# Optimization experiments

Measured on AMD Instinct MI355X. Metric: run time of the kernel, lower is better.

## Reference

```python
import jax, jax.numpy as jnp
import numpy as np

B, N, DIM = 2, 2048, 1024
HEADS, DIM_HEAD = 8, 64
INNER = HEADS * DIM_HEAD  # 512
EPS = 1e-5  # fp32 branch of the source LayerNorm


def setup_inputs() -> dict:
    key = jax.random.key(0)
    ks = jax.random.split(key, 5)
    x = jax.random.normal(ks[0], (B, N, DIM), dtype=jnp.float32)
    g = jnp.ones((DIM,), dtype=jnp.float32)  # LayerNorm gain init
    # Linear weights stored as (in, out) so y = x @ W. Source zero-inits
    # to_out; we use small random values so the baseline output is nonzero.
    wq = jax.random.normal(ks[1], (DIM, INNER), dtype=jnp.float32) * 0.02
    wkv = jax.random.normal(ks[2], (DIM, 2 * INNER), dtype=jnp.float32) * 0.02
    wo = jax.random.normal(ks[3], (INNER, DIM), dtype=jnp.float32) * 0.02
    return {"x": x, "g": g, "wq": wq, "wkv": wkv, "wo": wo}


def reference(x, g, wq, wkv, wo):
    # Custom LayerNorm from the source: statistics over dim=1 (sequence axis!)
    mean = jnp.mean(x, axis=1, keepdims=True)
    var = jnp.var(x, axis=1, keepdims=True)  # unbiased=False
    xn = (x - mean) * jax.lax.rsqrt(var + EPS) * g  # g broadcasts on last dim

    q = xn @ wq                      # [b, n, inner]
    kv = xn @ wkv                    # [b, n, 2*inner]
    k, v = jnp.split(kv, 2, axis=-1)

    def split_heads(t):  # b n (h d) -> b h n d
        b, n, _ = t.shape
        return t.reshape(b, n, HEADS, DIM_HEAD).transpose(0, 2, 1, 3)

    q, k, v = map(split_heads, (q, k, v))
    q = q * (DIM_HEAD ** -0.5)

    sim = jnp.einsum('bhid,bhjd->bhij', q, k)   # [b, h, n, n]
    attn = jax.nn.softmax(sim, axis=-1)
    out = jnp.einsum('bhij,bhjd->bhid', attn, v)  # [b, h, n, d]

    out = out.transpose(0, 2, 1, 3).reshape(B, N, INNER)  # b h n d -> b n (h d)
    return out @ wo  # [b, n, dim]
```

## Files before the change

### kernel.cpp

```cpp
#include <hip/hip_runtime.h>
#include <hip/hip_bf16.h>
#include <stdint.h>


#define B_ 2
#define N_ 2048
#define DIM_ 1024
#define DH_ 64
#define INNER_ 512
#define ROWS_ 4096
#define POSTRIDE 2097152
#define BHSTRIDE 131072

#define QSCALE 0.18033688011112042f

typedef __bf16 bf16x8 __attribute__((ext_vector_type(8)));
typedef float floatx4 __attribute__((ext_vector_type(4)));

#if __has_builtin(__builtin_amdgcn_exp2f)
#define EXP2(x) __builtin_amdgcn_exp2f(x)
#else
#define EXP2(x) exp2f(x)
#endif

__device__ __forceinline__ ushort f2bf(float f) {
    union { float f; uint32_t u; } v; v.f = f;
    uint32_t u = v.u;
    u += 0x7fffu + ((u >> 16) & 1u);
    return (ushort)(u >> 16);
}
__device__ __forceinline__ uint32_t pkbf(float a, float b) {
    return (uint32_t)f2bf(a) | ((uint32_t)f2bf(b) << 16);
}
__device__ __forceinline__ size_t frag_off(int m, int k, int nkc) {
    return ((size_t)((m >> 4) * nkc + (k >> 5)) * 64 +
            (size_t)((m & 15) | (((k >> 3) & 3) << 4))) * 8 + (k & 7);
}

__global__ __launch_bounds__(256) void setup_fused(
    const float* __restrict__ x, float* __restrict__ ps, float* __restrict__ pq,
    const float* __restrict__ wq, const float* __restrict__ wkv,
    const float* __restrict__ wo, ushort* __restrict__ wqkv_f,
    ushort* __restrict__ wo_f) {
    __shared__ float tile[32][33];
    int bid = blockIdx.x;
    if (bid < 256) {
        int gd = (bid & 7) * 256 + threadIdx.x;
        int ch = bid >> 3;
        int b = gd >> 10;
        const float* p = x + (size_t)(b * N_ + ch * 64) * DIM_ + (gd & 1023);
        float s = 0.f, q = 0.f;
#pragma unroll 4
        for (int n = 0; n < 64; ++n) { float v = p[(size_t)n * DIM_]; s += v; q += v * v; }
        ps[ch * 2048 + gd] = s;
        pq[ch * 2048 + gd] = q;
        return;
    }
    int t = bid - 256;
    const float* src; ushort* dst; int C, K, k0, ncol0, nglob0; float scale;
    if (t < 512) {
        int kt = t >> 4, nt = t & 15;
        src = wq; dst = wqkv_f; C = 512; K = 1024; scale = QSCALE;
        k0 = kt * 32; ncol0 = nt * 32; nglob0 = ncol0;
    } else if (t < 1536) {
        int u = t - 512; int kt = u >> 5, nt = u & 31;
        src = wkv; dst = wqkv_f; C = 1024; K = 1024; scale = 1.f;
        k0 = kt * 32; ncol0 = nt * 32; nglob0 = 512 + ncol0;
    } else {
        int u = t - 1536; int kt = u >> 5, nt = u & 31;
        src = wo; dst = wo_f; C = 1024; K = 512; scale = 1.f;
        k0 = kt * 32; ncol0 = nt * 32; nglob0 = ncol0;
    }
    int ti = threadIdx.x >> 5, tj = threadIdx.x & 31;
#pragma unroll
    for (int p = 0; p < 4; ++p)
        tile[ti + 8 * p][tj] = src[(size_t)(k0 + ti + 8 * p) * C + ncol0 + tj] * scale;
    __syncthreads();
    if (threadIdx.x < 128) {
        int nl = threadIdx.x & 31, kc8 = threadIdx.x >> 5;
        union { ushort us[8]; uint4 v; } u;
#pragma unroll
        for (int ii = 0; ii < 8; ++ii) u.us[ii] = f2bf(tile[kc8 * 8 + ii][nl]);
        *(uint4*)&dst[frag_off(nglob0 + nl, k0 + kc8 * 8, K >> 5)] = u.v;
    }
}

__global__ __launch_bounds__(256) void finalize_norm(
    const float* __restrict__ ps, const float* __restrict__ pq,
    const float* __restrict__ x, const float* __restrict__ g,
    ushort* __restrict__ xnf) {
    __shared__ float s4[4][64], q4[4][64], aa[64], bb[64];
    int t = threadIdx.x;
    int b = blockIdx.x >> 8, slab = (blockIdx.x >> 4) & 15, nch = blockIdx.x & 15;
    int c0 = slab * 64;
    {
        int c = t & 63, grp = t >> 6;
        float s = 0.f, q = 0.f;
#pragma unroll
        for (int ch = 0; ch < 8; ++ch) {
            int o = (grp * 8 + ch) * 2048 + b * 1024 + c0 + c;
            s += ps[o]; q += pq[o];
        }
        s4[grp][c] = s; q4[grp][c] = q;
    }
    __syncthreads();
    if (t < 64) {
        float s = s4[0][t] + s4[1][t] + s4[2][t] + s4[3][t];
        float q = q4[0][t] + q4[1][t] + q4[2][t] + q4[3][t];
        float mean = s * (1.f / N_);
        float var = q * (1.f / N_) - mean * mean;
        float rstd = rsqrtf(var + 1e-5f);
        float a = rstd * g[c0 + t];
        aa[t] = a; bb[t] = -mean * a;
    }
    __syncthreads();
    int c4 = (t & 15) * 4, ro = t >> 4;
#pragma unroll
    for (int it = 0; it < 8; ++it) {
        int r = nch * 128 + it * 16 + ro;
        int m = b * 2048 + r;
        float4 xv = *(const float4*)&x[(size_t)m * DIM_ + c0 + c4];
        float v0 = xv.x * aa[c4 + 0] + bb[c4 + 0];
        float v1 = xv.y * aa[c4 + 1] + bb[c4 + 1];
        float v2 = xv.z * aa[c4 + 2] + bb[c4 + 2];
        float v3 = xv.w * aa[c4 + 3] + bb[c4 + 3];
        uint2 u; u.x = pkbf(v0, v1); u.y = pkbf(v2, v3);
        *(uint2*)&xnf[frag_off(m, c0 + c4, 32)] = u;
    }
}

template <int NKC>
__device__ __forceinline__ void gemm_core(
    const ushort* __restrict__ pA, const ushort* __restrict__ pB,
    floatx4 (&acc)[4][4]) {
    constexpr int TS = NKC * 512;
    bf16x8 a0[4], b0[4], a1[4], b1[4];
#pragma unroll
    for (int i = 0; i < 4; ++i) {
        a0[i] = *(const bf16x8*)(pA + (size_t)i * TS);
        b0[i] = *(const bf16x8*)(pB + (size_t)i * TS);
    }
    for (int kc = 0; kc < NKC; kc += 2) {
#pragma unroll
        for (int i = 0; i < 4; ++i) {
            a1[i] = *(const bf16x8*)(pA + (size_t)i * TS + (size_t)(kc + 1) * 512);
            b1[i] = *(const bf16x8*)(pB + (size_t)i * TS + (size_t)(kc + 1) * 512);
        }
#pragma unroll
        for (int mi = 0; mi < 4; ++mi)
#pragma unroll
            for (int ni = 0; ni < 4; ++ni)
                acc[mi][ni] = __builtin_amdgcn_mfma_f32_16x16x32_bf16(
                    a0[mi], b0[ni], acc[mi][ni], 0, 0, 0);
        if (kc + 2 < NKC) {
#pragma unroll
            for (int i = 0; i < 4; ++i) {
                a0[i] = *(const bf16x8*)(pA + (size_t)i * TS + (size_t)(kc + 2) * 512);
                b0[i] = *(const bf16x8*)(pB + (size_t)i * TS + (size_t)(kc + 2) * 512);
            }
        }
#pragma unroll
        for (int mi = 0; mi < 4; ++mi)
#pragma unroll
            for (int ni = 0; ni < 4; ++ni)
                acc[mi][ni] = __builtin_amdgcn_mfma_f32_16x16x32_bf16(
                    a1[mi], b1[ni], acc[mi][ni], 0, 0, 0);
    }
}

__global__ __launch_bounds__(128) void gemm_qkv(
    const ushort* __restrict__ xnf, const ushort* __restrict__ wf,
    ushort* __restrict__ qf, ushort* __restrict__ kf, ushort* __restrict__ vf) {
    int tx = threadIdx.x, w = tx >> 6, l = tx & 63;
    int lr = l & 15, lq = l >> 4;
    int bx = blockIdx.x, by = blockIdx.y;
    const ushort* pA = xnf + (size_t)(bx * 4) * 32 * 512 + l * 8;
    const ushort* pB = wf + (size_t)(by * 8 + w * 4) * 32 * 512 + l * 8;
    floatx4 acc[4][4] = {};
    gemm_core<32>(pA, pB, acc);
    int col0 = by * 128 + w * 64;
    int bb2 = (bx * 64) >> 11;
    if (by < 8) {
        ushort* qkbase = (by < 4) ? qf : kf;
#pragma unroll
        for (int ni = 0; ni < 4; ++ni) {
            int col = col0 + 16 * ni + lr;
            int hh = (col >> 6) & 7, d = col & 63;
            ushort* base = qkbase + (size_t)(bb2 * 8 + hh) * BHSTRIDE
                           + (d >> 5) * 512 + ((d >> 3) & 3) * 128 + (d & 7)
                           + (4 * lq) * 8;
#pragma unroll
            for (int mi = 0; mi < 4; ++mi) {
                size_t o2 = (size_t)((bx * 4 + mi) & 127) * 1024;
#pragma unroll
                for (int reg = 0; reg < 4; ++reg)
                    base[o2 + reg * 8] = f2bf(acc[mi][ni][reg]);
            }
        }
    } else {
#pragma unroll
        for (int ni = 0; ni < 4; ++ni) {
            int cv = col0 - 1024 + 16 * ni + lr;
            int hh = cv >> 6, d = cv & 63;
            ushort* base = vf + (size_t)(bb2 * 8 + hh) * BHSTRIDE
                           + (d >> 4) * 32768 + (d & 15) * 8;
#pragma unroll
            for (int mi = 0; mi < 4; ++mi) {
                int nn = (bx * 64 + 16 * mi + 4 * lq) & 2047;
                uint2 u;
                u.x = pkbf(acc[mi][ni][0], acc[mi][ni][1]);
                u.y = pkbf(acc[mi][ni][2], acc[mi][ni][3]);
                *(uint2*)&base[(nn >> 5) * 512 + ((nn >> 3) & 3) * 128 + (nn & 7)] = u;
            }
        }
    }
}

__global__ __launch_bounds__(128) void gemm_out(
    const ushort* __restrict__ af, const ushort* __restrict__ wf,
    float* __restrict__ out) {
    int tx = threadIdx.x, w = tx >> 6, l = tx & 63;
    int lr = l & 15, lq = l >> 4;
    int bx = blockIdx.x, by = blockIdx.y;
    const ushort* pA = af + (size_t)(bx * 4) * 16 * 512 + l * 8;
    const ushort* pB = wf + (size_t)(by * 8 + w * 4) * 16 * 512 + l * 8;
    floatx4 acc[4][4] = {};
    gemm_core<16>(pA, pB, acc);
    int col0 = by * 128 + w * 64;
#pragma unroll
    for (int mi = 0; mi < 4; ++mi)
#pragma unroll
        for (int ni = 0; ni < 4; ++ni) {
            int col = col0 + 16 * ni + lr;
#pragma unroll
            for (int reg = 0; reg < 4; ++reg) {
                int row = bx * 64 + 16 * mi + 4 * lq + reg;
                out[(size_t)row * 1024 + col] = acc[mi][ni][reg];
            }
        }
}

__global__ __launch_bounds__(256, 2) void flash_attn(
    const ushort* __restrict__ qf, const ushort* __restrict__ kf,
    const ushort* __restrict__ vf, float* __restrict__ po,
    float* __restrict__ pl, int nkt) {
    __shared__ __align__(16) ushort sP[4][64 * 72];

    const int tx = threadIdx.x;
    const int w = tx >> 6, l = tx & 63;
    const int lr = l & 15, lq = l >> 4;
    const int qt = blockIdx.x, bh = blockIdx.y, sp = blockIdx.z;
    const int qbase = qt * 256 + w * 64;

    const ushort* qfb = qf + (size_t)bh * BHSTRIDE + (size_t)(qt * 16 + w * 4) * 1024 + l * 8;
    const ushort* kfb = kf + (size_t)bh * BHSTRIDE + (size_t)(sp * nkt * 4) * 1024 + l * 8;
    const ushort* vfb = vf + (size_t)bh * BHSTRIDE + (size_t)(sp * nkt * 2) * 512 + l * 8;
    ushort* sPw = &sP[w][0];

    bf16x8 bq[4][2];
#pragma unroll
    for (int qq = 0; qq < 4; ++qq)
#pragma unroll
        for (int s = 0; s < 2; ++s)
            bq[qq][s] = *(const bf16x8*)(qfb + qq * 1024 + s * 512);

    floatx4 o[4][4] = {};
    float lsum[4] = {0.f, 0.f, 0.f, 0.f};

    bf16x8 ak[8], bv[8];
#pragma unroll
    for (int kk = 0; kk < 4; ++kk) {
        ak[kk * 2 + 0] = *(const bf16x8*)(kfb + kk * 1024);
        ak[kk * 2 + 1] = *(const bf16x8*)(kfb + kk * 1024 + 512);
    }

    for (int kt = 0; kt < nkt; ++kt) {
#pragma unroll
        for (int dt = 0; dt < 4; ++dt) {
            bv[dt * 2 + 0] = *(const bf16x8*)(vfb + dt * 32768 + (kt * 2 + 0) * 512);
            bv[dt * 2 + 1] = *(const bf16x8*)(vfb + dt * 32768 + (kt * 2 + 1) * 512);
        }

        floatx4 c[4][4] = {};
#pragma unroll
        for (int s = 0; s < 2; ++s)
#pragma unroll
            for (int kk = 0; kk < 4; ++kk)
#pragma unroll
                for (int qq = 0; qq < 4; ++qq)
                    c[kk][qq] = __builtin_amdgcn_mfma_f32_16x16x32_bf16(
                        ak[kk * 2 + s], bq[qq][s], c[kk][qq], 0, 0, 0);

        if (kt + 1 < nkt) {
            const ushort* kp = kfb + (size_t)(kt + 1) * 4096;
#pragma unroll
            for (int kk = 0; kk < 4; ++kk) {
                ak[kk * 2 + 0] = *(const bf16x8*)(kp + kk * 1024);
                ak[kk * 2 + 1] = *(const bf16x8*)(kp + kk * 1024 + 512);
            }
        }

#pragma unroll
        for (int kk = 0; kk < 4; ++kk)
#pragma unroll
            for (int qq = 0; qq < 4; ++qq) {
                float e0 = EXP2(c[kk][qq][0]);
                float e1 = EXP2(c[kk][qq][1]);
                float e2 = EXP2(c[kk][qq][2]);
                float e3 = EXP2(c[kk][qq][3]);
                lsum[qq] += (e0 + e1) + (e2 + e3);
                uint2 u; u.x = pkbf(e0, e1); u.y = pkbf(e2, e3);
                *(uint2*)&sPw[(16 * qq + lr) * 72 + 16 * kk + 4 * lq] = u;
            }

#pragma unroll
        for (int s = 0; s < 2; ++s) {
            bf16x8 ap[4];
#pragma unroll
            for (int mi = 0; mi < 4; ++mi)
                ap[mi] = *(const bf16x8*)&sPw[(16 * mi + lr) * 72 + 32 * s + 8 * lq];
#pragma unroll
            for (int mi = 0; mi < 4; ++mi)
#pragma unroll
                for (int dt = 0; dt < 4; ++dt)
                    o[mi][dt] = __builtin_amdgcn_mfma_f32_16x16x32_bf16(
                        ap[mi], bv[dt * 2 + s], o[mi][dt], 0, 0, 0);
        }
    }

#pragma unroll
    for (int qq = 0; qq < 4; ++qq) {
        lsum[qq] += __shfl_xor(lsum[qq], 16);
        lsum[qq] += __shfl_xor(lsum[qq], 32);
    }
    float* pob = po + (size_t)sp * POSTRIDE;
    if (lq == 0) {
#pragma unroll
        for (int qq = 0; qq < 4; ++qq)
            pl[((size_t)sp * 16 + bh) * N_ + qbase + 16 * qq + lr] = lsum[qq];
    }
    const size_t obase = (size_t)bh * N_;
#pragma unroll
    for (int mi = 0; mi < 4; ++mi)
#pragma unroll
        for (int dt = 0; dt < 4; ++dt)
#pragma unroll
            for (int reg = 0; reg < 4; ++reg) {
                int row = qbase + 16 * mi + 4 * lq + reg;
                pob[(obase + row) * DH_ + 16 * dt + lr] = o[mi][dt][reg];
            }
}

__global__ __launch_bounds__(256) void merge_attn(
    const float* __restrict__ po, const float* __restrict__ pl,
    ushort* __restrict__ attnf, int nsplit) {
    int idx = blockIdx.x * 256 + threadIdx.x;
    int d4 = (idx & 15) * 4;
    int h = (idx >> 4) & 7;
    int rowg = idx >> 7;
    int b = rowg >> 11, r = rowg & 2047;
    size_t pbase = ((size_t)b * 8 + h) * N_ + r;
    float4 acc = *(const float4*)&po[pbase * DH_ + d4];
    float lv = pl[pbase];
    for (int s = 1; s < nsplit; ++s) {
        float4 a1 = *(const float4*)&po[(size_t)s * POSTRIDE + pbase * DH_ + d4];
        acc.x += a1.x; acc.y += a1.y; acc.z += a1.z; acc.w += a1.w;
        lv += pl[((size_t)s * 16) * N_ + pbase];
    }
    float inv = 1.f / lv;
    uint2 u;
    u.x = pkbf(acc.x * inv, acc.y * inv);
    u.y = pkbf(acc.z * inv, acc.w * inv);
    *(uint2*)&attnf[frag_off(rowg, h * DH_ + d4, 16)] = u;
}

extern "C" void kernel_launch(void* const* d_in, const int* in_sizes, int n_in,
                              void* d_out, int out_size, void* d_ws, size_t ws_size,
                              hipStream_t stream) {
    const float* x   = (const float*)d_in[0];
    const float* g   = (const float*)d_in[1];
    const float* wq  = (const float*)d_in[2];
    const float* wkv = (const float*)d_in[3];
    const float* wo  = (const float*)d_in[4];
    float* out = (float*)d_out;

    char* ws = (char*)d_ws;
    float*  psum   = (float*)(ws + 0);
    float*  psqr   = (float*)(ws + 262144);
    ushort* xnf    = (ushort*)(ws + 524288);
    ushort* wqkv_f = (ushort*)(ws + 8912896);
    ushort* wo_f   = (ushort*)(ws + 12058624);
    ushort* qfb    = (ushort*)(ws + 13107200);
    ushort* kfb    = (ushort*)(ws + 17301504);
    ushort* vfb    = (ushort*)(ws + 21495808);
    ushort* attnf  = (ushort*)(ws + 25690112);
    float*  plb    = (float*)(ws + 29884416);
    float*  pob    = (float*)(ws + 30408704);

    const int nsplit = (ws_size >= (size_t)66 * 1024 * 1024) ? 4
                     : (ws_size >= (size_t)48 * 1024 * 1024) ? 2 : 1;

    setup_fused<<<2304, 256, 0, stream>>>(x, psum, psqr, wq, wkv, wo, wqkv_f, wo_f);
    finalize_norm<<<512, 256, 0, stream>>>(psum, psqr, x, g, xnf);
    gemm_qkv<<<dim3(64, 12), 128, 0, stream>>>(xnf, wqkv_f, qfb, kfb, vfb);
    flash_attn<<<dim3(8, 16, nsplit), 256, 0, stream>>>(qfb, kfb, vfb, pob, plb, 32 / nsplit);
    merge_attn<<<2048, 256, 0, stream>>>(pob, plb, attnf, nsplit);
    gemm_out<<<dim3(64, 8), 128, 0, stream>>>(attnf, wo_f, out);
}
```

Baseline: 163.2 us.

## Split KV across waves inside flash block and merge partials in LDS

The flash attention kernel now gives each of its four waves a quarter of the key range for the same 64 queries, instead of giving each wave its own query rows and splitting keys across a grid dimension. The partial outputs and row sums are reduced through shared memory and written straight out as normalized bf16, so the separate merge kernel and its fp32 partial buffers in global memory are gone. The GEMM and attention grids are also flattened, with block IDs remapped so that neighbouring tiles land on the same XCD for better L2 reuse. The cost is a larger LDS footprint and a block-wide sync, and each block now does less MFMA work for more reduction overhead.

```diff
diff --git a/kernel.cpp b/kernel.cpp
--- a/kernel.cpp
+++ b/kernel.cpp
@@ -9,7 +9,6 @@
 #define DH_ 64
 #define INNER_ 512
 #define ROWS_ 4096
-#define POSTRIDE 2097152
 #define BHSTRIDE 131072
 
 #define QSCALE 0.18033688011112042f
@@ -173,7 +172,10 @@
     ushort* __restrict__ qf, ushort* __restrict__ kf, ushort* __restrict__ vf) {
     int tx = threadIdx.x, w = tx >> 6, l = tx & 63;
     int lr = l & 15, lq = l >> 4;
-    int bx = blockIdx.x, by = blockIdx.y;
+    int bid = blockIdx.x;
+    int xcd = bid & 7, t = bid >> 3;
+    int bx = xcd * 8 + (t & 7);
+    int by = t >> 3;
     const ushort* pA = xnf + (size_t)(bx * 4) * 32 * 512 + l * 8;
     const ushort* pB = wf + (size_t)(by * 8 + w * 4) * 32 * 512 + l * 8;
     floatx4 acc[4][4] = {};
@@ -221,7 +223,10 @@
     float* __restrict__ out) {
     int tx = threadIdx.x, w = tx >> 6, l = tx & 63;
     int lr = l & 15, lq = l >> 4;
-    int bx = blockIdx.x, by = blockIdx.y;
+    int bid = blockIdx.x;
+    int xcd = bid & 7, t = bid >> 3;
+    int bx = xcd * 8 + (t & 7);
+    int by = t >> 3;
     const ushort* pA = af + (size_t)(bx * 4) * 16 * 512 + l * 8;
     const ushort* pB = wf + (size_t)(by * 8 + w * 4) * 16 * 512 + l * 8;
     floatx4 acc[4][4] = {};
@@ -242,20 +247,21 @@
 
 __global__ __launch_bounds__(256, 2) void flash_attn(
     const ushort* __restrict__ qf, const ushort* __restrict__ kf,
-    const ushort* __restrict__ vf, float* __restrict__ po,
-    float* __restrict__ pl, int nkt) {
-    __shared__ __align__(16) ushort sP[4][64 * 72];
+    const ushort* __restrict__ vf, ushort* __restrict__ attnf) {
+    __shared__ __align__(16) float sArena[4 * 4352];
+    __shared__ float sL[4][64];
 
     const int tx = threadIdx.x;
     const int w = tx >> 6, l = tx & 63;
     const int lr = l & 15, lq = l >> 4;
-    const int qt = blockIdx.x, bh = blockIdx.y, sp = blockIdx.z;
-    const int qbase = qt * 256 + w * 64;
-
-    const ushort* qfb = qf + (size_t)bh * BHSTRIDE + (size_t)(qt * 16 + w * 4) * 1024 + l * 8;
-    const ushort* kfb = kf + (size_t)bh * BHSTRIDE + (size_t)(sp * nkt * 4) * 1024 + l * 8;
-    const ushort* vfb = vf + (size_t)bh * BHSTRIDE + (size_t)(sp * nkt * 2) * 512 + l * 8;
-    ushort* sPw = &sP[w][0];
+    const int bid = blockIdx.x;
+    const int bh = (bid & 7) * 2 + ((bid >> 3) & 1);
+    const int qt = bid >> 4;
+
+    const ushort* qfb = qf + (size_t)bh * BHSTRIDE + (size_t)(qt * 4) * 1024 + l * 8;
+    const ushort* kfb = kf + (size_t)bh * BHSTRIDE + (size_t)w * 32768 + l * 8;
+    const ushort* vfb = vf + (size_t)bh * BHSTRIDE + (size_t)w * 8192 + l * 8;
+    ushort* sPw = (ushort*)(sArena + w * 4352);
 
     bf16x8 bq[4][2];
 #pragma unroll
@@ -274,7 +280,7 @@
         ak[kk * 2 + 1] = *(const bf16x8*)(kfb + kk * 1024 + 512);
     }
 
-    for (int kt = 0; kt < nkt; ++kt) {
+    for (int kt = 0; kt < 8; ++kt) {
 #pragma unroll
         for (int dt = 0; dt < 4; ++dt) {
             bv[dt * 2 + 0] = *(const bf16x8*)(vfb + dt * 32768 + (kt * 2 + 0) * 512);
@@ -291,7 +297,7 @@
                     c[kk][qq] = __builtin_amdgcn_mfma_f32_16x16x32_bf16(
                         ak[kk * 2 + s], bq[qq][s], c[kk][qq], 0, 0, 0);
 
-        if (kt + 1 < nkt) {
+        if (kt + 1 < 8) {
             const ushort* kp = kfb + (size_t)(kt + 1) * 4096;
 #pragma unroll
             for (int kk = 0; kk < 4; ++kk) {
@@ -333,45 +339,45 @@
         lsum[qq] += __shfl_xor(lsum[qq], 16);
         lsum[qq] += __shfl_xor(lsum[qq], 32);
     }
-    float* pob = po + (size_t)sp * POSTRIDE;
+
+    float* Rw = sArena + w * 4352;
+#pragma unroll
+    for (int mi = 0; mi < 4; ++mi)
+#pragma unroll
+        for (int dt = 0; dt < 4; ++dt)
+#pragma unroll
+            for (int reg = 0; reg < 4; ++reg)
+                Rw[(16 * mi + 4 * lq + reg) * 68 + 16 * dt + lr] = o[mi][dt][reg];
     if (lq == 0) {
 #pragma unroll
-        for (int qq = 0; qq < 4; ++qq)
-            pl[((size_t)sp * 16 + bh) * N_ + qbase + 16 * qq + lr] = lsum[qq];
-    }
-    const size_t obase = (size_t)bh * N_;
-#pragma unroll
-    for (int mi = 0; mi < 4; ++mi)
-#pragma unroll
-        for (int dt = 0; dt < 4; ++dt)
-#pragma unroll
-            for (int reg = 0; reg < 4; ++reg) {
-                int row = qbase + 16 * mi + 4 * lq + reg;
-                pob[(obase + row) * DH_ + 16 * dt + lr] = o[mi][dt][reg];
-            }
-}
-
-__global__ __launch_bounds__(256) void merge_attn(
-    const float* __restrict__ po, const float* __restrict__ pl,
-    ushort* __restrict__ attnf, int nsplit) {
-    int idx = blockIdx.x * 256 + threadIdx.x;
-    int d4 = (idx & 15) * 4;
-    int h = (idx >> 4) & 7;
-    int rowg = idx >> 7;
-    int b = rowg >> 11, r = rowg & 2047;
-    size_t pbase = ((size_t)b * 8 + h) * N_ + r;
-    float4 acc = *(const float4*)&po[pbase * DH_ + d4];
-    float lv = pl[pbase];
-    for (int s = 1; s < nsplit; ++s) {
-        float4 a1 = *(const float4*)&po[(size_t)s * POSTRIDE + pbase * DH_ + d4];
-        acc.x += a1.x; acc.y += a1.y; acc.z += a1.z; acc.w += a1.w;
-        lv += pl[((size_t)s * 16) * N_ + pbase];
-    }
-    float inv = 1.f / lv;
-    uint2 u;
-    u.x = pkbf(acc.x * inv, acc.y * inv);
-    u.y = pkbf(acc.z * inv, acc.w * inv);
-    *(uint2*)&attnf[frag_off(rowg, h * DH_ + d4, 16)] = u;
+        for (int qq = 0; qq < 4; ++qq) sL[w][16 * qq + lr] = lsum[qq];
+    }
+    __syncthreads();
+
+    int qloc = 16 * w + (l >> 2);
+    int c0 = (l & 3) * 16;
+    float4 acc[4];
+#pragma unroll
+    for (int rg = 0; rg < 4; ++rg) {
+        const float* R = sArena + rg * 4352 + qloc * 68 + c0;
+#pragma unroll
+        for (int c = 0; c < 4; ++c) {
+            float4 v = *(const float4*)&R[4 * c];
+            if (rg == 0) acc[c] = v;
+            else { acc[c].x += v.x; acc[c].y += v.y; acc[c].z += v.z; acc[c].w += v.w; }
+        }
+    }
+    float ltot = sL[0][qloc] + sL[1][qloc] + sL[2][qloc] + sL[3][qloc];
+    float inv = 1.f / ltot;
+    int m = (bh >> 3) * 2048 + qt * 64 + qloc;
+    int kb = (bh & 7) * 64 + c0;
+#pragma unroll
+    for (int c = 0; c < 4; ++c) {
+        uint2 u;
+        u.x = pkbf(acc[c].x * inv, acc[c].y * inv);
+        u.y = pkbf(acc[c].z * inv, acc[c].w * inv);
+        *(uint2*)&attnf[frag_off(m, kb + 4 * c, 16)] = u;
+    }
 }
 
 extern "C" void kernel_launch(void* const* d_in, const int* in_sizes, int n_in,
@@ -394,16 +400,10 @@
     ushort* kfb    = (ushort*)(ws + 17301504);
     ushort* vfb    = (ushort*)(ws + 21495808);
     ushort* attnf  = (ushort*)(ws + 25690112);
-    float*  plb    = (float*)(ws + 29884416);
-    float*  pob    = (float*)(ws + 30408704);
-
-    const int nsplit = (ws_size >= (size_t)66 * 1024 * 1024) ? 4
-                     : (ws_size >= (size_t)48 * 1024 * 1024) ? 2 : 1;
 
     setup_fused<<<2304, 256, 0, stream>>>(x, psum, psqr, wq, wkv, wo, wqkv_f, wo_f);
     finalize_norm<<<512, 256, 0, stream>>>(psum, psqr, x, g, xnf);
-    gemm_qkv<<<dim3(64, 12), 128, 0, stream>>>(xnf, wqkv_f, qfb, kfb, vfb);
-    flash_attn<<<dim3(8, 16, nsplit), 256, 0, stream>>>(qfb, kfb, vfb, pob, plb, 32 / nsplit);
-    merge_attn<<<2048, 256, 0, stream>>>(pob, plb, attnf, nsplit);
-    gemm_out<<<dim3(64, 8), 128, 0, stream>>>(attnf, wo_f, out);
-}
+    gemm_qkv<<<768, 128, 0, stream>>>(xnf, wqkv_f, qfb, kfb, vfb);
+    flash_attn<<<512, 256, 0, stream>>>(qfb, kfb, vfb, attnf);
+    gemm_out<<<512, 128, 0, stream>>>(attnf, wo_f, out);
+}
```

After: 147.3 us (median of 2 runs). 1.11x faster.
